# Optimization experiments

Hardware: AMD Instinct MI355X
Metric: run time of the kernel (lower is better)

Reference implementation:

```python
import jax, jax.numpy as jnp
import numpy as np

HEADS = 8
KSIZE = 3


def _unfold(t, ksize):
    # t: [B, C, H, W] -> [B, C, k*k, H, W], zero padding k//2, stride 1
    B, C, H, W = t.shape
    pad = ksize // 2
    tp = jnp.pad(t, ((0, 0), (0, 0), (pad, pad), (pad, pad)))
    patches = [tp[:, :, i:i + H, j:j + W] for i in range(ksize) for j in range(ksize)]
    return jnp.stack(patches, axis=2)


def setup_inputs() -> dict:
    key = jax.random.key(0)
    k0, k1, k2, k3 = jax.random.split(key, 4)
    B, C, H, W = 2, 256, 96, 96
    x = jax.random.normal(k0, (B, C, H, W), dtype=jnp.float32)
    w_qkv = jax.random.normal(k1, (3 * C, C), dtype=jnp.float32) * 0.02  # 1x1 conv, no bias
    w_out = jax.random.normal(k2, (C, C), dtype=jnp.float32) * 0.02     # 1x1 conv
    b_out = jax.random.normal(k3, (C,), dtype=jnp.float32) * 0.02
    return {"x": x, "w_qkv": w_qkv, "w_out": w_out, "b_out": b_out}


def reference(x, w_qkv, w_out, b_out):
    B, C, H, W = x.shape
    hd = C // HEADS
    scale = hd ** (-0.5)
    kk = KSIZE * KSIZE

    qkv = jnp.einsum('bchw,oc->bohw', x, w_qkv)          # [B, 3C, H, W]
    q, k, v = jnp.split(qkv, 3, axis=1)
    # unfold -> [B, heads, C/heads, k^2, H, W]
    q, k, v = [_unfold(t, KSIZE).reshape(B, HEADS, hd, kk, H, W) for t in (q, k, v)]

    # contract over the k^2 window dim (s); n,m are the per-head channel dims
    dots = jnp.einsum('bhnsij,bhmsij->bhnmij', q * scale, k)  # [B,h,hd,hd,H,W]
    attn = jax.nn.softmax(dots, axis=3)                       # softmax over m (dim=-3)
    out = jnp.einsum('bhnmij,bhmsij->bhnsij', attn, v)        # [B,h,hd,k^2,H,W]
    out = out.reshape(B, C, kk, H, W).sum(axis=2)             # [B,C,H,W]
    out = jnp.einsum('bchw,oc->bohw', out, w_out) + b_out[None, :, None, None] + x
    return out
```

## Files before the change

### kernel.cpp

```cpp
#include <hip/hip_runtime.h>

#define H96 96
#define W96 96
#define HW  9216
#define NC  256
#define NB  2
#define NHEADS 8
#define HD  32
#define SCALE 0.17677669529663687f

typedef __attribute__((ext_vector_type(8))) short short8v;
typedef __attribute__((ext_vector_type(4))) float f32x4;
typedef __attribute__((ext_vector_type(16))) float f32x16;

__device__ __forceinline__ ushort f2bf(float f) {
    unsigned u = __float_as_uint(f);
    u += 0x7FFFu + ((u >> 16) & 1u);
    return (ushort)(u >> 16);
}
__device__ __forceinline__ float bf2f(ushort h) {
    return __uint_as_float(((unsigned)h) << 16);
}

__global__ __launch_bounds__(256)
void x_to_bf16t(const float* __restrict__ x, ushort* __restrict__ xt,
                ushort* __restrict__ xbm)
{
    __shared__ float tile[32][33];
    const int t = threadIdx.x;
    const int hw0 = blockIdx.x * 32, c0 = blockIdx.y * 32, b = blockIdx.z;

    const int r = t >> 3, cc = (t & 7) * 4;
    const size_t gidx = ((size_t)b * NC + c0 + r) * HW + hw0 + cc;
    const float4 v = *(const float4*)(x + gidx);
    tile[r][cc + 0] = v.x; tile[r][cc + 1] = v.y; tile[r][cc + 2] = v.z; tile[r][cc + 3] = v.w;
    ushort4 ob;
    ob.x = f2bf(v.x); ob.y = f2bf(v.y); ob.z = f2bf(v.z); ob.w = f2bf(v.w);
    *(ushort4*)(xbm + gidx) = ob;
    __syncthreads();

    const int hwr = t >> 3, c4 = (t & 7) * 4;
    ushort4 o;
    o.x = f2bf(tile[c4 + 0][hwr]);
    o.y = f2bf(tile[c4 + 1][hwr]);
    o.z = f2bf(tile[c4 + 2][hwr]);
    o.w = f2bf(tile[c4 + 3][hwr]);
    *(ushort4*)(xt + ((size_t)b * HW + hw0 + hwr) * NC + c0 + c4) = o;
}

__global__ __launch_bounds__(256)
void conv_w(const float* __restrict__ wq, const float* __restrict__ wo,
            ushort* __restrict__ oq, ushort* __restrict__ oo)
{
    const int bid = blockIdx.x;
    if (bid < 192) {
        const int i = (bid * 256 + threadIdx.x) * 4;
        const float s = (i < 65536) ? (SCALE * 1.4426950408889634f) : 1.0f;
        const float4 v = *(const float4*)(wq + i);
        ushort4 u;
        u.x = f2bf(v.x * s); u.y = f2bf(v.y * s); u.z = f2bf(v.z * s); u.w = f2bf(v.w * s);
        *(ushort4*)(oq + i) = u;
    } else {
        const int i = ((bid - 192) * 256 + threadIdx.x) * 4;
        const float4 v = *(const float4*)(wo + i);
        ushort4 u;
        u.x = f2bf(v.x); u.y = f2bf(v.y); u.z = f2bf(v.z); u.w = f2bf(v.w);
        *(ushort4*)(oo + i) = u;
    }
}

__device__ __forceinline__ void stage_tile(const ushort* __restrict__ g, ushort* lds,
                                           int w, int lane)
{
    const int lr  = lane >> 3;
    const int swz = ((lane & 7) ^ lr) * 8;
    #pragma unroll
    for (int ii = 0; ii < 4; ++ii) {
        const int rowbase = w * 32 + ii * 8;
        const ushort* src = g + (size_t)(rowbase + lr) * NC + swz;
        __builtin_amdgcn_global_load_lds((const __attribute__((address_space(1))) void*)src,
                                         (__attribute__((address_space(3))) void*)(lds + rowbase * 64),
                                         16, 0, 0);
    }
}

template<int EPI>
__global__ __launch_bounds__(256)
void gemm_mfma(const ushort* __restrict__ A, const ushort* __restrict__ Bt,
               void* __restrict__ Cout, const float* __restrict__ bias,
               const ushort* __restrict__ resb, int Mtot)
{
    __shared__ __align__(16) ushort smem[128 * 136];
    ushort* As = smem;
    ushort* Bs = smem + 128 * 64;

    const int t = threadIdx.x;
    const int lane = t & 63, w = t >> 6;
    const int wm = w >> 1, wn = w & 1;

    const int l = blockIdx.x;
    const int chunk = (EPI == 0) ? 108 : 36;
    const int mt    = (EPI == 0) ? 6 : 2;
    const int id2 = (l & 7) * chunk + (l >> 3);
    const int n_tile = id2 / mt;
    const int n0 = n_tile * 128;
    const int m0 = (id2 - n_tile * mt) * 128;

    const ushort* Ag = A + (size_t)m0 * NC;
    const ushort* Bg = Bt + (size_t)n0 * NC;

    f32x4 acc[4][4];
    #pragma unroll
    for (int i = 0; i < 4; ++i)
        #pragma unroll
        for (int j = 0; j < 4; ++j)
            acc[i][j] = (f32x4){0.f, 0.f, 0.f, 0.f};

    for (int k0 = 0; k0 < NC; k0 += 64) {
        stage_tile(Ag + k0, As, w, lane);
        stage_tile(Bg + k0, Bs, w, lane);
        __syncthreads();
        #pragma unroll
        for (int ks = 0; ks < 2; ++ks) {
            const int kc = (lane >> 4) + ks * 4;
            const int sw = (kc ^ (lane & 7)) * 8;
            short8v af[4], bf_[4];
            #pragma unroll
            for (int f = 0; f < 4; ++f) {
                af[f]  = *(const short8v*)(As + (wm * 64 + f * 16 + (lane & 15)) * 64 + sw);
                bf_[f] = *(const short8v*)(Bs + (wn * 64 + f * 16 + (lane & 15)) * 64 + sw);
            }
            #pragma unroll
            for (int fi = 0; fi < 4; ++fi)
                #pragma unroll
                for (int fj = 0; fj < 4; ++fj)
                    acc[fi][fj] = __builtin_amdgcn_mfma_f32_16x16x32_bf16(af[fi], bf_[fj], acc[fi][fj], 0, 0, 0);
        }
        __syncthreads();
    }

    const int b = n0 / HW;
    const int hw0 = n0 - b * HW;

    if constexpr (EPI == 0) {
        #pragma unroll
        for (int fi = 0; fi < 4; ++fi)
            #pragma unroll
            for (int fj = 0; fj < 4; ++fj) {
                const int hwl = wn * 64 + fj * 16 + (lane & 15);
                const int ml  = wm * 64 + fi * 16 + (lane >> 4) * 4;
                ushort4 v4;
                v4.x = f2bf(acc[fi][fj][0]);
                v4.y = f2bf(acc[fi][fj][1]);
                v4.z = f2bf(acc[fi][fj][2]);
                v4.w = f2bf(acc[fi][fj][3]);
                *(ushort4*)(smem + hwl * 136 + ml) = v4;
            }
        __syncthreads();
        ushort* C = (ushort*)Cout;
        #pragma unroll
        for (int it = 0; it < 8; ++it) {
            const int cid = it * 256 + t;
            const int hwl = cid >> 4, mc = (cid & 15) * 8;
            const uint4 v = *(const uint4*)(smem + hwl * 136 + mc);
            *(uint4*)(C + ((size_t)b * HW + hw0 + hwl) * (size_t)Mtot + m0 + mc) = v;
        }
    } else {
        float* C = (float*)Cout;
        const int ncol = hw0 + wn * 64 + (lane & 15);
        #pragma unroll
        for (int fi = 0; fi < 4; ++fi)
            #pragma unroll
            for (int r = 0; r < 4; ++r) {
                const int m = m0 + wm * 64 + fi * 16 + (lane >> 4) * 4 + r;
                const float bm = bias[m];
                const size_t base = ((size_t)b * NC + m) * HW + ncol;
                #pragma unroll
                for (int fj = 0; fj < 4; ++fj)
                    C[base + fj * 16] = acc[fi][fj][r] + bm + bf2f(resb[base + fj * 16]);
            }
    }
}

__global__ __launch_bounds__(256)
void attn_mfma(const ushort* __restrict__ qkvp, ushort* __restrict__ att)
{
    __shared__ ushort khT[32 * 74];
    __shared__ ushort qhT[32 * 74];
    __shared__ ushort vh[54 * 40];
    __shared__ float  vs[16 * 32];

    const int t = threadIdx.x;
    const int sraw = blockIdx.x;
    const int strip = (sraw & 7) * 72 + (sraw >> 3);
    const int h = blockIdx.y;
    const int b = blockIdx.z;
    const int i0 = strip / 6;
    const int j0 = (strip - (strip / 6) * 6) * 16;

    const ushort* P = qkvp + (size_t)b * HW * 768;
    const int qo = h * HD, ko = NC + h * HD, vo = 2 * NC + h * HD;

    for (int z = t; z < 640; z += 256) {
        const int arr = z & 1, rest = z >> 1;
        const int ch = rest & 31, rp = rest >> 5;
        ushort* dst = (arr ? qhT : khT) + ch * 74 + 54 + rp * 2;
        *(unsigned*)dst = 0u;
    }

    if (t < 216) {
        const int px = t >> 2, c8 = (t & 3) * 8;
        const int dy = px / 18, dx = px - dy * 18;
        const int gi = i0 - 1 + dy, gj = j0 - 1 + dx;
        uint4 qv = {0, 0, 0, 0}, kv = {0, 0, 0, 0}, vv = {0, 0, 0, 0};
        if (gi >= 0 && gi < H96 && gj >= 0 && gj < W96) {
            const ushort* pp = P + ((size_t)gi * W96 + gj) * 768;
            qv = *(const uint4*)(pp + qo + c8);
            kv = *(const uint4*)(pp + ko + c8);
            vv = *(const uint4*)(pp + vo + c8);
        }
        *(uint4*)(vh + px * 40 + c8) = vv;
        const unsigned ku[4] = {kv.x, kv.y, kv.z, kv.w};
        const unsigned qu[4] = {qv.x, qv.y, qv.z, qv.w};
        #pragma unroll
        for (int i = 0; i < 4; ++i) {
            khT[(c8 + 2 * i)     * 74 + px] = (ushort)(ku[i] & 0xFFFFu);
            khT[(c8 + 2 * i + 1) * 74 + px] = (ushort)(ku[i] >> 16);
            qhT[(c8 + 2 * i)     * 74 + px] = (ushort)(qu[i] & 0xFFFFu);
            qhT[(c8 + 2 * i + 1) * 74 + px] = (ushort)(qu[i] >> 16);
        }
    }
    __syncthreads();

    {
        const int px = t >> 4, m2 = (t & 15) * 2;
        float a0 = 0.f, a1 = 0.f;
        #pragma unroll
        for (int dy = 0; dy < 3; ++dy)
            #pragma unroll
            for (int dx = 0; dx < 3; ++dx) {
                const ushort* pv = vh + (dy * 18 + px + dx) * 40 + m2;
                a0 += bf2f(pv[0]);
                a1 += bf2f(pv[1]);
            }
        vs[px * 32 + m2]     = a0;
        vs[px * 32 + m2 + 1] = a1;
    }
    __syncthreads();

    const int lane = t & 63, w = t >> 6;
    const int hi = lane >> 5, ch = lane & 31;
    const ushort* kb = khT + ch * 74 + hi * 36;
    const ushort* qb = qhT + ch * 74 + hi * 36;

    #pragma unroll
    for (int p = 0; p < 4; ++p) {
        const int c = w * 4 + p;

        unsigned kk0, kk1, kk2, kk3, qq0, qq1, qq2, qq3;
        if ((p & 1) == 0) {
            kk0 = *(const unsigned*)(kb + c);      kk1 = *(const unsigned*)(kb + c + 2);
            kk2 = *(const unsigned*)(kb + c + 18); kk3 = *(const unsigned*)(kb + c + 20);
            qq0 = *(const unsigned*)(qb + c);
            qq1 = *(const unsigned*)(qb + c + 2)  & 0x0000FFFFu;
            qq2 = *(const unsigned*)(qb + c + 18);
            qq3 = *(const unsigned*)(qb + c + 20) & 0x0000FFFFu;
        } else {
            kk0 = *(const unsigned*)(kb + c - 1);  kk1 = *(const unsigned*)(kb + c + 1);
            kk2 = *(const unsigned*)(kb + c + 17); kk3 = *(const unsigned*)(kb + c + 19);
            qq0 = *(const unsigned*)(qb + c - 1)  & 0xFFFF0000u;
            qq1 = *(const unsigned*)(qb + c + 1);
            qq2 = *(const unsigned*)(qb + c + 17) & 0xFFFF0000u;
            qq3 = *(const unsigned*)(qb + c + 19);
        }

        union { unsigned u[4]; short8v v; } A_, B_;
        A_.u[0] = kk0; A_.u[1] = kk1; A_.u[2] = kk2; A_.u[3] = kk3;
        B_.u[0] = qq0; B_.u[1] = qq1; B_.u[2] = qq2; B_.u[3] = qq3;

        f32x16 dm;
        #pragma unroll
        for (int r = 0; r < 16; ++r) dm[r] = 0.f;
        dm = __builtin_amdgcn_mfma_f32_32x32x16_bf16(A_.v, B_.v, dm, 0, 0, 0);

        float vsv[16];
        #pragma unroll
        for (int g = 0; g < 4; ++g) {
            const float4 vv = *(const float4*)(vs + c * 32 + g * 8 + hi * 4);
            vsv[g * 4 + 0] = vv.x; vsv[g * 4 + 1] = vv.y;
            vsv[g * 4 + 2] = vv.z; vsv[g * 4 + 3] = vv.w;
        }

        float sum = 0.f, out = 0.f;
        #pragma unroll
        for (int r = 0; r < 16; ++r) {
            const float pe = __builtin_amdgcn_exp2f(dm[r]);
            sum += pe;
            out = fmaf(pe, vsv[r], out);
        }
        sum += __shfl_xor(sum, 32);
        out += __shfl_xor(out, 32);

        if (hi == 0) {
            const float inv = __builtin_amdgcn_rcpf(sum);
            att[((size_t)b * HW + (size_t)i0 * W96 + j0 + c) * NC + h * HD + ch] =
                f2bf(out * inv);
        }
    }
}

extern "C" void kernel_launch(void* const* d_in, const int* in_sizes, int n_in,
                              void* d_out, int out_size, void* d_ws, size_t ws_size,
                              hipStream_t stream)
{
    (void)in_sizes; (void)n_in; (void)out_size; (void)ws_size;
    const float* x     = (const float*)d_in[0];
    const float* w_qkv = (const float*)d_in[1];
    const float* w_out = (const float*)d_in[2];
    const float* b_out = (const float*)d_in[3];
    float* out = (float*)d_out;

    ushort* qkvp = (ushort*)d_ws;
    ushort* attb = qkvp + (size_t)NB * HW * 768;
    ushort* xt   = attb + (size_t)NB * HW * NC;
    ushort* wqb  = xt   + (size_t)NB * HW * NC;
    ushort* wob  = wqb  + 768 * NC;
    ushort* xbm  = wob  + NC * NC;

    x_to_bf16t<<<dim3(HW / 32, NC / 32, NB), 256, 0, stream>>>(x, xt, xbm);
    conv_w<<<dim3(256), 256, 0, stream>>>(w_qkv, w_out, wqb, wob);
    gemm_mfma<0><<<dim3(864), 256, 0, stream>>>(wqb, xt, qkvp, nullptr, nullptr, 768);
    attn_mfma<<<dim3(576, NHEADS, NB), 256, 0, stream>>>(qkvp, attb);
    gemm_mfma<1><<<dim3(288), 256, 0, stream>>>(wob, attb, out, b_out, xbm, 256);
}
```

Before: 140.8 us.

## Process two output rows per attention block to share halo loads

Each attention block now covers a 2x16 pixel tile instead of 1x16, so the 4x18 halo of q/k/v is loaded once for two rows, and the grid is halved. Q/K transposes are written as packed 32-bit pairs, and the V window sum is vectorized to four channels per thread. Each wave now runs eight MFMA iterations instead of four, and the upper half-wave zeroes its second-row operands instead of loading them. The aim is less redundant global traffic and fewer scalar LDS stores per output, at the cost of more work per block and fewer blocks in flight.

```diff
diff --git a/kernel.cpp b/kernel.cpp
--- a/kernel.cpp
+++ b/kernel.cpp
@@ -187,91 +187,103 @@
 {
     __shared__ ushort khT[32 * 74];
     __shared__ ushort qhT[32 * 74];
-    __shared__ ushort vh[54 * 40];
-    __shared__ float  vs[16 * 32];
+    __shared__ ushort vh[72 * 40];
+    __shared__ float  vs[32 * 32];
 
     const int t = threadIdx.x;
     const int sraw = blockIdx.x;
-    const int strip = (sraw & 7) * 72 + (sraw >> 3);
+    const int s = (sraw & 7) * 36 + (sraw >> 3);
     const int h = blockIdx.y;
     const int b = blockIdx.z;
-    const int i0 = strip / 6;
-    const int j0 = (strip - (strip / 6) * 6) * 16;
+    const int I0 = (s / 6) * 2;
+    const int j0 = (s - (s / 6) * 6) * 16;
 
     const ushort* P = qkvp + (size_t)b * HW * 768;
     const int qo = h * HD, ko = NC + h * HD, vo = 2 * NC + h * HD;
 
-    for (int z = t; z < 640; z += 256) {
-        const int arr = z & 1, rest = z >> 1;
-        const int ch = rest & 31, rp = rest >> 5;
-        ushort* dst = (arr ? qhT : khT) + ch * 74 + 54 + rp * 2;
-        *(unsigned*)dst = 0u;
-    }
-
-    if (t < 216) {
-        const int px = t >> 2, c8 = (t & 3) * 8;
-        const int dy = px / 18, dx = px - dy * 18;
-        const int gi = i0 - 1 + dy, gj = j0 - 1 + dx;
-        uint4 qv = {0, 0, 0, 0}, kv = {0, 0, 0, 0}, vv = {0, 0, 0, 0};
-        if (gi >= 0 && gi < H96 && gj >= 0 && gj < W96) {
-            const ushort* pp = P + ((size_t)gi * W96 + gj) * 768;
-            qv = *(const uint4*)(pp + qo + c8);
-            kv = *(const uint4*)(pp + ko + c8);
-            vv = *(const uint4*)(pp + vo + c8);
-        }
-        *(uint4*)(vh + px * 40 + c8) = vv;
-        const unsigned ku[4] = {kv.x, kv.y, kv.z, kv.w};
-        const unsigned qu[4] = {qv.x, qv.y, qv.z, qv.w};
-        #pragma unroll
-        for (int i = 0; i < 4; ++i) {
-            khT[(c8 + 2 * i)     * 74 + px] = (ushort)(ku[i] & 0xFFFFu);
-            khT[(c8 + 2 * i + 1) * 74 + px] = (ushort)(ku[i] >> 16);
-            qhT[(c8 + 2 * i)     * 74 + px] = (ushort)(qu[i] & 0xFFFFu);
-            qhT[(c8 + 2 * i + 1) * 74 + px] = (ushort)(qu[i] >> 16);
+    for (int z = t; z < 576; z += 256) {
+        if (z < 288) {
+            const int arr = z & 1, chunk = (z >> 1) & 3, pair = z >> 3;
+            const int px0 = pair * 2;
+            const int hy = px0 / 18, hx = px0 - hy * 18;
+            const int gi = I0 - 1 + hy, gj = j0 - 1 + hx;
+            const int off = (arr ? ko : qo) + chunk * 8;
+            uint4 v0 = {0, 0, 0, 0}, v1 = {0, 0, 0, 0};
+            if (gi >= 0 && gi < H96) {
+                const ushort* pr = P + (size_t)gi * W96 * 768 + off;
+                if (gj >= 0 && gj < W96) v0 = *(const uint4*)(pr + (size_t)gj * 768);
+                if (gj + 1 < W96)        v1 = *(const uint4*)(pr + (size_t)(gj + 1) * 768);
+            }
+            ushort* dst = (arr ? khT : qhT) + (chunk * 8) * 74 + px0;
+            const unsigned a0[4] = {v0.x, v0.y, v0.z, v0.w};
+            const unsigned a1[4] = {v1.x, v1.y, v1.z, v1.w};
+            #pragma unroll
+            for (int i = 0; i < 4; ++i) {
+                *(unsigned*)(dst + (2 * i) * 74)     = (a0[i] & 0xFFFFu) | (a1[i] << 16);
+                *(unsigned*)(dst + (2 * i + 1) * 74) = (a0[i] >> 16) | (a1[i] & 0xFFFF0000u);
+            }
+        } else {
+            const int u = z - 288;
+            const int px = u >> 2, chunk = u & 3;
+            const int hy = px / 18, hx = px - hy * 18;
+            const int gi = I0 - 1 + hy, gj = j0 - 1 + hx;
+            uint4 vv = {0, 0, 0, 0};
+            if (gi >= 0 && gi < H96 && gj >= 0 && gj < W96)
+                vv = *(const uint4*)(P + ((size_t)gi * W96 + gj) * 768 + vo + chunk * 8);
+            *(uint4*)(vh + px * 40 + chunk * 8) = vv;
         }
     }
     __syncthreads();
 
     {
-        const int px = t >> 4, m2 = (t & 15) * 2;
-        float a0 = 0.f, a1 = 0.f;
+        const int px = t >> 3, q4 = (t & 7) * 4;
+        const int r = px >> 4, c = px & 15;
+        float a0 = 0.f, a1 = 0.f, a2 = 0.f, a3 = 0.f;
         #pragma unroll
         for (int dy = 0; dy < 3; ++dy)
             #pragma unroll
             for (int dx = 0; dx < 3; ++dx) {
-                const ushort* pv = vh + (dy * 18 + px + dx) * 40 + m2;
-                a0 += bf2f(pv[0]);
-                a1 += bf2f(pv[1]);
-            }
-        vs[px * 32 + m2]     = a0;
-        vs[px * 32 + m2 + 1] = a1;
+                const ushort4 u4 = *(const ushort4*)(vh + ((r + dy) * 18 + c + dx) * 40 + q4);
+                a0 += bf2f(u4.x); a1 += bf2f(u4.y); a2 += bf2f(u4.z); a3 += bf2f(u4.w);
+            }
+        *(float4*)(vs + px * 32 + q4) = (float4){a0, a1, a2, a3};
     }
     __syncthreads();
 
     const int lane = t & 63, w = t >> 6;
     const int hi = lane >> 5, ch = lane & 31;
-    const ushort* kb = khT + ch * 74 + hi * 36;
-    const ushort* qb = qhT + ch * 74 + hi * 36;
+    const int rw = w >> 1;
+    const int cbase = (w & 1) * 8;
+    const ushort* kb = khT + ch * 74 + hi * 36 + rw * 18;
+    const ushort* qb = qhT + ch * 74 + hi * 36 + rw * 18;
 
     #pragma unroll
-    for (int p = 0; p < 4; ++p) {
-        const int c = w * 4 + p;
+    for (int p = 0; p < 8; ++p) {
+        const int c = cbase + p;
 
         unsigned kk0, kk1, kk2, kk3, qq0, qq1, qq2, qq3;
         if ((p & 1) == 0) {
-            kk0 = *(const unsigned*)(kb + c);      kk1 = *(const unsigned*)(kb + c + 2);
-            kk2 = *(const unsigned*)(kb + c + 18); kk3 = *(const unsigned*)(kb + c + 20);
+            kk0 = *(const unsigned*)(kb + c);
+            kk1 = *(const unsigned*)(kb + c + 2);
             qq0 = *(const unsigned*)(qb + c);
-            qq1 = *(const unsigned*)(qb + c + 2)  & 0x0000FFFFu;
-            qq2 = *(const unsigned*)(qb + c + 18);
-            qq3 = *(const unsigned*)(qb + c + 20) & 0x0000FFFFu;
+            qq1 = *(const unsigned*)(qb + c + 2) & 0x0000FFFFu;
+            if (hi == 0) {
+                kk2 = *(const unsigned*)(kb + c + 18);
+                kk3 = *(const unsigned*)(kb + c + 20);
+                qq2 = *(const unsigned*)(qb + c + 18);
+                qq3 = *(const unsigned*)(qb + c + 20) & 0x0000FFFFu;
+            } else { kk2 = kk3 = qq2 = qq3 = 0u; }
         } else {
-            kk0 = *(const unsigned*)(kb + c - 1);  kk1 = *(const unsigned*)(kb + c + 1);
-            kk2 = *(const unsigned*)(kb + c + 17); kk3 = *(const unsigned*)(kb + c + 19);
-            qq0 = *(const unsigned*)(qb + c - 1)  & 0xFFFF0000u;
+            kk0 = *(const unsigned*)(kb + c - 1);
+            kk1 = *(const unsigned*)(kb + c + 1);
+            qq0 = *(const unsigned*)(qb + c - 1) & 0xFFFF0000u;
             qq1 = *(const unsigned*)(qb + c + 1);
-            qq2 = *(const unsigned*)(qb + c + 17) & 0xFFFF0000u;
-            qq3 = *(const unsigned*)(qb + c + 19);
+            if (hi == 0) {
+                kk2 = *(const unsigned*)(kb + c + 17);
+                kk3 = *(const unsigned*)(kb + c + 19);
+                qq2 = *(const unsigned*)(qb + c + 17) & 0xFFFF0000u;
+                qq3 = *(const unsigned*)(qb + c + 19);
+            } else { kk2 = kk3 = qq2 = qq3 = 0u; }
         }
 
         union { unsigned u[4]; short8v v; } A_, B_;
@@ -283,10 +295,11 @@
         for (int r = 0; r < 16; ++r) dm[r] = 0.f;
         dm = __builtin_amdgcn_mfma_f32_32x32x16_bf16(A_.v, B_.v, dm, 0, 0, 0);
 
+        const int pxc = rw * 16 + c;
         float vsv[16];
         #pragma unroll
         for (int g = 0; g < 4; ++g) {
-            const float4 vv = *(const float4*)(vs + c * 32 + g * 8 + hi * 4);
+            const float4 vv = *(const float4*)(vs + pxc * 32 + g * 8 + hi * 4);
             vsv[g * 4 + 0] = vv.x; vsv[g * 4 + 1] = vv.y;
             vsv[g * 4 + 2] = vv.z; vsv[g * 4 + 3] = vv.w;
         }
@@ -303,7 +316,7 @@
 
         if (hi == 0) {
             const float inv = __builtin_amdgcn_rcpf(sum);
-            att[((size_t)b * HW + (size_t)i0 * W96 + j0 + c) * NC + h * HD + ch] =
+            att[((size_t)b * HW + (size_t)(I0 + rw) * W96 + j0 + c) * NC + h * HD + ch] =
                 f2bf(out * inv);
         }
     }
@@ -330,6 +343,6 @@
     x_to_bf16t<<<dim3(HW / 32, NC / 32, NB), 256, 0, stream>>>(x, xt, xbm);
     conv_w<<<dim3(256), 256, 0, stream>>>(w_qkv, w_out, wqb, wob);
     gemm_mfma<0><<<dim3(864), 256, 0, stream>>>(wqb, xt, qkvp, nullptr, nullptr, 768);
-    attn_mfma<<<dim3(576, NHEADS, NB), 256, 0, stream>>>(qkvp, attb);
+    attn_mfma<<<dim3(288, NHEADS, NB), 256, 0, stream>>>(qkvp, attb);
     gemm_mfma<1><<<dim3(288), 256, 0, stream>>>(wob, attb, out, b_out, xbm, 256);
 }
```

Result: slower. 145.0 us (+2.9%).
